# Performance work log

Measured on AMD Instinct MI355X. Metric: run time of the kernel, lower is better.

## Reference

```python
import jax, jax.numpy as jnp
import numpy as np

HID = 16

def _lrconv(x, edge_index, edge_attr, w1, b1, w2, b2):
    # flow='target_to_source': x_i = x[edge_index[0]], x_j = x[edge_index[1]],
    # aggregate (max) at edge_index[0].
    src = edge_index[0]
    dst = edge_index[1]
    m = jnp.concatenate([x[src], x[dst], edge_attr], axis=-1)  # [E, 2*in+edge]
    m = jax.nn.relu(m @ w1 + b1)
    m = jax.nn.relu(m @ w2 + b2)  # [E, out], all >= 0
    agg = jax.ops.segment_max(m, src, num_segments=x.shape[0])
    # empty segments get -inf in jax; PyG fills with 0. Messages are ReLU'd (>=0),
    # so clamping at 0 is exact.
    return jnp.maximum(agg, 0.0)

def _glorot(key, shape):
    fan_in, fan_out = shape
    lim = float(np.sqrt(6.0 / (fan_in + fan_out)))
    return jax.random.uniform(key, shape, jnp.float32, -lim, lim)

def setup_inputs() -> dict:
    key = jax.random.key(0)
    ks = jax.random.split(key, 16)
    N, E = 100000, 1600000
    x = jax.random.normal(ks[0], (N, 4), jnp.float32)
    edge_index = jax.random.randint(ks[1], (2, E), 0, N, jnp.int64)
    edge_attr = jax.random.normal(ks[2], (E, 8), jnp.float32)
    # conv1: in=4 -> cat dim 4*2+8=16
    c1_w1 = _glorot(ks[3], (16, HID)); c1_b1 = jnp.zeros((HID,), jnp.float32)
    c1_w2 = _glorot(ks[4], (HID, 16)); c1_b2 = jnp.zeros((16,), jnp.float32)
    # conv2: in=16 -> cat dim 16*2+8=40
    c2_w1 = _glorot(ks[5], (40, HID)); c2_b1 = jnp.zeros((HID,), jnp.float32)
    c2_w2 = _glorot(ks[6], (HID, 16)); c2_b2 = jnp.zeros((16,), jnp.float32)
    l1_w = _glorot(ks[7], (16, 16)); l1_b = jnp.zeros((16,), jnp.float32)
    l2_w = _glorot(ks[8], (16, 1)); l2_b = jnp.zeros((1,), jnp.float32)
    return {"x": x, "edge_index": edge_index, "edge_attr": edge_attr,
            "c1_w1": c1_w1, "c1_b1": c1_b1, "c1_w2": c1_w2, "c1_b2": c1_b2,
            "c2_w1": c2_w1, "c2_b1": c2_b1, "c2_w2": c2_w2, "c2_b2": c2_b2,
            "l1_w": l1_w, "l1_b": l1_b, "l2_w": l2_w, "l2_b": l2_b}

def reference(x, edge_index, edge_attr,
              c1_w1, c1_b1, c1_w2, c1_b2,
              c2_w1, c2_b1, c2_w2, c2_b2,
              l1_w, l1_b, l2_w, l2_b):
    h = _lrconv(x, edge_index, edge_attr, c1_w1, c1_b1, c1_w2, c1_b2)   # [N,16]
    h = _lrconv(h, edge_index, edge_attr, c2_w1, c2_b1, c2_w2, c2_b2)   # [N,16]
    h = jax.nn.relu(h @ l1_w + l1_b)
    return h @ l2_w + l2_b  # [N,1]
```

## Files before the change

### kernel.cpp

```cpp
#include <hip/hip_runtime.h>
#include <hip/hip_fp16.h>

#define CHUNK 1024

typedef _Float16 half8 __attribute__((ext_vector_type(8)));
typedef float floatx4 __attribute__((ext_vector_type(4)));

__device__ __forceinline__ unsigned int pack2(float a, float b) {
    __half2 h = __floats2half2_rn(a, b);
    return *(unsigned int*)&h;
}
__device__ __forceinline__ float2 unpack2(unsigned int u) {
    __half2 h = *(__half2*)&u;
    return __half22float2(h);
}

__global__ __launch_bounds__(256) void rank_cvt(
    const int* __restrict__ ei, const float* __restrict__ ea,
    int* __restrict__ deg, unsigned short* __restrict__ r,
    _Float16* __restrict__ eah, int E)
{
    int e = blockIdx.x * 256 + threadIdx.x;
    if (e >= E) return;
    r[e] = (unsigned short)atomicAdd(&deg[ei[e]], 1);
    float4 a0 = *(const float4*)(ea + (size_t)e * 8);
    float4 a1 = *(const float4*)(ea + (size_t)e * 8 + 4);
    half8 h;
    h[0] = (_Float16)a0.x; h[1] = (_Float16)a0.y;
    h[2] = (_Float16)a0.z; h[3] = (_Float16)a0.w;
    h[4] = (_Float16)a1.x; h[5] = (_Float16)a1.y;
    h[6] = (_Float16)a1.z; h[7] = (_Float16)a1.w;
    *(half8*)(eah + (size_t)e * 8) = h;
}

__global__ __launch_bounds__(256) void scan_chunk_sums(
    const int* __restrict__ v, int* __restrict__ csum, int N)
{
    __shared__ int s[256];
    int base = blockIdx.x * CHUNK;
    int t = threadIdx.x;
    int acc = 0;
    #pragma unroll
    for (int i = 0; i < CHUNK / 256; ++i) {
        int idx = base + t + i * 256;
        if (idx < N) acc += v[idx];
    }
    s[t] = acc; __syncthreads();
    for (int o = 128; o > 0; o >>= 1) {
        if (t < o) s[t] += s[t + o];
        __syncthreads();
    }
    if (t == 0) csum[blockIdx.x] = s[0];
}

__global__ void scan_chunk_off(
    const int* __restrict__ csum, int* __restrict__ coff, int nch)
{
    if (threadIdx.x == 0 && blockIdx.x == 0) {
        int acc = 0;
        for (int i = 0; i < nch; ++i) { coff[i] = acc; acc += csum[i]; }
    }
}

__global__ __launch_bounds__(256) void scan_within_excl(
    const int* __restrict__ deg, int* __restrict__ pos,
    const int* __restrict__ coff, int N)
{
    __shared__ int s[256];
    int t = threadIdx.x;
    int base = blockIdx.x * CHUNK + t * 4;
    int v0 = 0, v1 = 0, v2 = 0, v3 = 0;
    if (base + 0 < N) v0 = deg[base + 0];
    if (base + 1 < N) v1 = deg[base + 1];
    if (base + 2 < N) v2 = deg[base + 2];
    if (base + 3 < N) v3 = deg[base + 3];
    s[t] = v0 + v1 + v2 + v3;
    __syncthreads();
    for (int o = 1; o < 256; o <<= 1) {
        int add = (t >= o) ? s[t - o] : 0;
        __syncthreads();
        s[t] += add;
        __syncthreads();
    }
    int run = coff[blockIdx.x] + (t > 0 ? s[t - 1] : 0);
    if (base + 0 < N) pos[base + 0] = run; run += v0;
    if (base + 1 < N) pos[base + 1] = run; run += v1;
    if (base + 2 < N) pos[base + 2] = run; run += v2;
    if (base + 3 < N) pos[base + 3] = run;
}

__global__ __launch_bounds__(256) void edge_mlp1(
    const float* __restrict__ x,
    const int*   __restrict__ ei,
    const _Float16* __restrict__ eah,
    const int*   __restrict__ pos,
    const unsigned short* __restrict__ r,
    const float* __restrict__ w1, const float* __restrict__ b1,
    const float* __restrict__ w2, const float* __restrict__ b2,
    _Float16* __restrict__ m2h,
    int E)
{
    __shared__ _Float16 itm[4][4][16][24];
    __shared__ int      sd[4][2][64];
    int tid = threadIdx.x;
    int w = tid >> 6, lane = tid & 63;
    int e16 = lane & 15, q = lane >> 4;

    half8 B1, B2;
    #pragma unroll
    for (int j = 0; j < 8; ++j) { B1[j] = (_Float16)0.f; B2[j] = (_Float16)0.f; }
    if (q < 2) {
        #pragma unroll
        for (int j = 0; j < 8; ++j) {
            B1[j] = (_Float16)w1[(8 * q + j) * 16 + e16];
            B2[j] = (_Float16)w2[(8 * q + j) * 16 + e16];
        }
    }
    float b1c = b1[e16], b2c = b2[e16];

    int wid = blockIdx.x * 4 + w;
    int nw  = gridDim.x * 4;
    int ntiles = (E + 63) >> 6;

    for (int tile = wid; tile < ntiles; tile += nw) {
        int ebase = tile << 6;
        int e = ebase + lane;
        int s_l = 0, d_l = 0, p_l = 0;
        if (e < E) {
            s_l = ei[e];
            d_l = ei[E + e];
            p_l = pos[s_l] + (int)r[e];
        }
        sd[w][0][lane] = s_l;
        sd[w][1][lane] = d_l;
        __builtin_amdgcn_wave_barrier();

        half8 A[4];
        #pragma unroll
        for (int t = 0; t < 4; ++t) {
            half8 a;
            #pragma unroll
            for (int j = 0; j < 8; ++j) a[j] = (_Float16)0.f;
            int et = ebase + 16 * t + e16;
            if (q == 0 && et < E) {
                int s = sd[w][0][16 * t + e16];
                int d = sd[w][1][16 * t + e16];
                float4 xs = *(const float4*)(x + (size_t)s * 4);
                float4 xd = *(const float4*)(x + (size_t)d * 4);
                a[0] = (_Float16)xs.x; a[1] = (_Float16)xs.y;
                a[2] = (_Float16)xs.z; a[3] = (_Float16)xs.w;
                a[4] = (_Float16)xd.x; a[5] = (_Float16)xd.y;
                a[6] = (_Float16)xd.z; a[7] = (_Float16)xd.w;
            } else if (q == 1 && et < E) {
                a = *(const half8*)(eah + (size_t)et * 8);
            }
            A[t] = a;
        }

        floatx4 C[4];
        #pragma unroll
        for (int t = 0; t < 4; ++t) {
            floatx4 c = {b1c, b1c, b1c, b1c};
            C[t] = __builtin_amdgcn_mfma_f32_16x16x32_f16(A[t], B1, c, 0, 0, 0);
        }
        #pragma unroll
        for (int t = 0; t < 4; ++t)
            #pragma unroll
            for (int i = 0; i < 4; ++i)
                itm[w][t][4 * q + i][e16] = (_Float16)fmaxf(C[t][i], 0.0f);
        __builtin_amdgcn_wave_barrier();

        half8 A2[4];
        #pragma unroll
        for (int t = 0; t < 4; ++t) {
            half8 a;
            #pragma unroll
            for (int j = 0; j < 8; ++j) a[j] = (_Float16)0.f;
            if (q < 2) a = *(const half8*)&itm[w][t][e16][8 * q];
            A2[t] = a;
        }
        __builtin_amdgcn_wave_barrier();
        floatx4 C2[4];
        #pragma unroll
        for (int t = 0; t < 4; ++t) {
            floatx4 c = {b2c, b2c, b2c, b2c};
            C2[t] = __builtin_amdgcn_mfma_f32_16x16x32_f16(A2[t], B2, c, 0, 0, 0);
        }
        #pragma unroll
        for (int t = 0; t < 4; ++t)
            #pragma unroll
            for (int i = 0; i < 4; ++i)
                itm[w][t][4 * q + i][e16] = (_Float16)C2[t][i];
        __builtin_amdgcn_wave_barrier();

        if (e < E) {
            half8 lo = *(const half8*)&itm[w][q][e16][0];
            half8 hi = *(const half8*)&itm[w][q][e16][8];
            *(half8*)(m2h + (size_t)p_l * 16)     = lo;
            *(half8*)(m2h + (size_t)p_l * 16 + 8) = hi;
        }
        __builtin_amdgcn_wave_barrier();
    }
}

__global__ __launch_bounds__(256) void edge_mlp2(
    const float* __restrict__ hw_s,
    const unsigned short* __restrict__ hw_dh,
    const int*   __restrict__ ei,
    const _Float16* __restrict__ eah,
    const int*   __restrict__ pos,
    const unsigned short* __restrict__ r,
    const float* __restrict__ w1,
    const float* __restrict__ w2, const float* __restrict__ b2,
    _Float16* __restrict__ m2h, int E)
{
    __shared__ _Float16 itm[4][4][16][24];
    __shared__ int      sd[4][2][64];
    int tid = threadIdx.x;
    int w = tid >> 6, lane = tid & 63;
    int e16 = lane & 15, q = lane >> 4;
    const __half* hwd = (const __half*)hw_dh;

    half8 B1, B2;
    #pragma unroll
    for (int j = 0; j < 8; ++j) { B1[j] = (_Float16)0.f; B2[j] = (_Float16)0.f; }
    if (q == 0) {
        #pragma unroll
        for (int j = 0; j < 8; ++j)
            B1[j] = (_Float16)w1[(32 + j) * 16 + e16];
    }
    if (q < 2) {
        #pragma unroll
        for (int j = 0; j < 8; ++j)
            B2[j] = (_Float16)w2[(8 * q + j) * 16 + e16];
    }
    float b2c = b2[e16];

    int wid = blockIdx.x * 4 + w;
    int nw  = gridDim.x * 4;
    int ntiles = (E + 63) >> 6;

    for (int tile = wid; tile < ntiles; tile += nw) {
        int ebase = tile << 6;
        int e = ebase + lane;
        int s_l = 0, d_l = 0, p_l = 0;
        if (e < E) {
            s_l = ei[e];
            d_l = ei[E + e];
            p_l = pos[s_l] + (int)r[e];
        }
        sd[w][0][lane] = s_l;
        sd[w][1][lane] = d_l;
        __builtin_amdgcn_wave_barrier();

        half8 A[4];
        #pragma unroll
        for (int t = 0; t < 4; ++t) {
            half8 a;
            #pragma unroll
            for (int j = 0; j < 8; ++j) a[j] = (_Float16)0.f;
            int et = ebase + 16 * t + e16;
            if (q == 0 && et < E)
                a = *(const half8*)(eah + (size_t)et * 8);
            A[t] = a;
        }

        floatx4 C[4];
        #pragma unroll
        for (int t = 0; t < 4; ++t) {
            floatx4 c;
            #pragma unroll
            for (int i = 0; i < 4; ++i) {
                int li = 16 * t + 4 * q + i;
                int rr = ebase + li;
                float v = 0.0f;
                if (rr < E) {
                    int s = sd[w][0][li];
                    int d = sd[w][1][li];
                    v = hw_s[(size_t)s * 16 + e16]
                      + __half2float(hwd[(size_t)d * 16 + e16]);
                }
                c[i] = v;
            }
            C[t] = __builtin_amdgcn_mfma_f32_16x16x32_f16(A[t], B1, c, 0, 0, 0);
        }
        #pragma unroll
        for (int t = 0; t < 4; ++t)
            #pragma unroll
            for (int i = 0; i < 4; ++i)
                itm[w][t][4 * q + i][e16] = (_Float16)fmaxf(C[t][i], 0.0f);
        __builtin_amdgcn_wave_barrier();

        half8 A2[4];
        #pragma unroll
        for (int t = 0; t < 4; ++t) {
            half8 a;
            #pragma unroll
            for (int j = 0; j < 8; ++j) a[j] = (_Float16)0.f;
            if (q < 2) a = *(const half8*)&itm[w][t][e16][8 * q];
            A2[t] = a;
        }
        __builtin_amdgcn_wave_barrier();
        floatx4 C2[4];
        #pragma unroll
        for (int t = 0; t < 4; ++t) {
            floatx4 c = {b2c, b2c, b2c, b2c};
            C2[t] = __builtin_amdgcn_mfma_f32_16x16x32_f16(A2[t], B2, c, 0, 0, 0);
        }
        #pragma unroll
        for (int t = 0; t < 4; ++t)
            #pragma unroll
            for (int i = 0; i < 4; ++i)
                itm[w][t][4 * q + i][e16] = (_Float16)C2[t][i];
        __builtin_amdgcn_wave_barrier();

        if (e < E) {
            half8 lo = *(const half8*)&itm[w][q][e16][0];
            half8 hi = *(const half8*)&itm[w][q][e16][8];
            *(half8*)(m2h + (size_t)p_l * 16)     = lo;
            *(half8*)(m2h + (size_t)p_l * 16 + 8) = hi;
        }
        __builtin_amdgcn_wave_barrier();
    }
}

__global__ __launch_bounds__(256) void segmax1_hw(
    const _Float16* __restrict__ m2h, const int* __restrict__ pos,
    const float* __restrict__ cw1, const float* __restrict__ cb1,
    float* __restrict__ hw_s, unsigned short* __restrict__ hw_dh,
    int N, int E)
{
    int tid = threadIdx.x;
    int n = blockIdx.x * 32 + (tid >> 3);
    if (n >= N) return;
    int g = tid & 7;
    int start = pos[n];
    int end = (n + 1 < N) ? pos[n + 1] : E;

    float acc[16];
    #pragma unroll
    for (int j = 0; j < 16; ++j) acc[j] = 0.0f;

    for (int k = start + g; k < end; k += 8) {
        uint4 u0 = *(const uint4*)(m2h + (size_t)k * 16);
        uint4 u1 = *(const uint4*)(m2h + (size_t)k * 16 + 8);
        float2 f;
        f = unpack2(u0.x); acc[0]  = fmaxf(acc[0],  f.x); acc[1]  = fmaxf(acc[1],  f.y);
        f = unpack2(u0.y); acc[2]  = fmaxf(acc[2],  f.x); acc[3]  = fmaxf(acc[3],  f.y);
        f = unpack2(u0.z); acc[4]  = fmaxf(acc[4],  f.x); acc[5]  = fmaxf(acc[5],  f.y);
        f = unpack2(u0.w); acc[6]  = fmaxf(acc[6],  f.x); acc[7]  = fmaxf(acc[7],  f.y);
        f = unpack2(u1.x); acc[8]  = fmaxf(acc[8],  f.x); acc[9]  = fmaxf(acc[9],  f.y);
        f = unpack2(u1.y); acc[10] = fmaxf(acc[10], f.x); acc[11] = fmaxf(acc[11], f.y);
        f = unpack2(u1.z); acc[12] = fmaxf(acc[12], f.x); acc[13] = fmaxf(acc[13], f.y);
        f = unpack2(u1.w); acc[14] = fmaxf(acc[14], f.x); acc[15] = fmaxf(acc[15], f.y);
    }
    #pragma unroll
    for (int mask = 1; mask < 8; mask <<= 1) {
        #pragma unroll
        for (int j = 0; j < 16; ++j)
            acc[j] = fmaxf(acc[j], __shfl_xor(acc[j], mask, 64));
    }

    int j0 = 2 * g, j1 = 2 * g + 1;
    float hs0 = cb1[j0], hs1 = cb1[j1], hd0 = 0.0f, hd1 = 0.0f;
    #pragma unroll
    for (int k = 0; k < 16; ++k) {
        float ak = acc[k];
        hs0 = fmaf(ak, cw1[k * 16 + j0], hs0);
        hs1 = fmaf(ak, cw1[k * 16 + j1], hs1);
        hd0 = fmaf(ak, cw1[(16 + k) * 16 + j0], hd0);
        hd1 = fmaf(ak, cw1[(16 + k) * 16 + j1], hd1);
    }
    *(float2*)(hw_s + (size_t)n * 16 + j0) = make_float2(hs0, hs1);
    ((unsigned int*)hw_dh)[(size_t)n * 8 + g] = pack2(hd0, hd1);
}

__global__ __launch_bounds__(256) void segmax2_head(
    const _Float16* __restrict__ m2h, const int* __restrict__ pos,
    const float* __restrict__ l1w, const float* __restrict__ l1b,
    const float* __restrict__ l2w, const float* __restrict__ l2b,
    float* __restrict__ out, int N, int E)
{
    int tid = threadIdx.x;
    int n = blockIdx.x * 32 + (tid >> 3);
    if (n >= N) return;
    int g = tid & 7;
    int start = pos[n];
    int end = (n + 1 < N) ? pos[n + 1] : E;

    float acc[16];
    #pragma unroll
    for (int j = 0; j < 16; ++j) acc[j] = 0.0f;

    for (int k = start + g; k < end; k += 8) {
        uint4 u0 = *(const uint4*)(m2h + (size_t)k * 16);
        uint4 u1 = *(const uint4*)(m2h + (size_t)k * 16 + 8);
        float2 f;
        f = unpack2(u0.x); acc[0]  = fmaxf(acc[0],  f.x); acc[1]  = fmaxf(acc[1],  f.y);
        f = unpack2(u0.y); acc[2]  = fmaxf(acc[2],  f.x); acc[3]  = fmaxf(acc[3],  f.y);
        f = unpack2(u0.z); acc[4]  = fmaxf(acc[4],  f.x); acc[5]  = fmaxf(acc[5],  f.y);
        f = unpack2(u0.w); acc[6]  = fmaxf(acc[6],  f.x); acc[7]  = fmaxf(acc[7],  f.y);
        f = unpack2(u1.x); acc[8]  = fmaxf(acc[8],  f.x); acc[9]  = fmaxf(acc[9],  f.y);
        f = unpack2(u1.y); acc[10] = fmaxf(acc[10], f.x); acc[11] = fmaxf(acc[11], f.y);
        f = unpack2(u1.z); acc[12] = fmaxf(acc[12], f.x); acc[13] = fmaxf(acc[13], f.y);
        f = unpack2(u1.w); acc[14] = fmaxf(acc[14], f.x); acc[15] = fmaxf(acc[15], f.y);
    }
    #pragma unroll
    for (int mask = 1; mask < 8; mask <<= 1) {
        #pragma unroll
        for (int j = 0; j < 16; ++j)
            acc[j] = fmaxf(acc[j], __shfl_xor(acc[j], mask, 64));
    }

    float t2[16];
    #pragma unroll
    for (int j = 0; j < 16; ++j) t2[j] = l1b[j];
    #pragma unroll
    for (int kk = 0; kk < 16; ++kk) {
        float ak = acc[kk];
        #pragma unroll
        for (int j = 0; j < 16; ++j) t2[j] = fmaf(ak, l1w[kk * 16 + j], t2[j]);
    }
    float r2 = l2b[0];
    #pragma unroll
    for (int j = 0; j < 16; ++j) r2 = fmaf(fmaxf(t2[j], 0.0f), l2w[j], r2);
    if (g == 0) out[n] = r2;
}

extern "C" void kernel_launch(void* const* d_in, const int* in_sizes, int n_in,
                              void* d_out, int out_size, void* d_ws, size_t ws_size,
                              hipStream_t stream)
{
    const float* x     = (const float*)d_in[0];
    const int*   ei    = (const int*)  d_in[1];
    const float* ea    = (const float*)d_in[2];
    const float* c1_w1 = (const float*)d_in[3];
    const float* c1_b1 = (const float*)d_in[4];
    const float* c1_w2 = (const float*)d_in[5];
    const float* c1_b2 = (const float*)d_in[6];
    const float* c2_w1 = (const float*)d_in[7];
    const float* c2_b1 = (const float*)d_in[8];
    const float* c2_w2 = (const float*)d_in[9];
    const float* c2_b2 = (const float*)d_in[10];
    const float* l1_w  = (const float*)d_in[11];
    const float* l1_b  = (const float*)d_in[12];
    const float* l2_w  = (const float*)d_in[13];
    const float* l2_b  = (const float*)d_in[14];
    float* out = (float*)d_out;

    const int N = in_sizes[0] / 4;
    const int E = in_sizes[2] / 8;
    const int nch = (N + CHUNK - 1) / CHUNK;

    const int BLK = 256;
    const int egrid = (E + BLK - 1) / BLK;
    const int ggrid = (N + 31) / 32;
    const int ntiles64 = (E + 63) >> 6;
    int mgrid = (ntiles64 + 15) / 16;
    if (mgrid < 256) mgrid = 256;

    size_t szN16f = (size_t)N * 16 * 4;
    size_t szN16h = (size_t)N * 16 * 2;
    size_t szN    = ((size_t)N * 4 + 15) & ~(size_t)15;
    size_t szEh   = ((size_t)E * 2 + 15) & ~(size_t)15;
    size_t szE16  = (size_t)E * 16;
    size_t szE32  = (size_t)E * 32;
    (void)szE32;

    size_t pos_off  = 0;
    size_t r_off    = pos_off  + szN;
    size_t hws_off  = r_off    + szEh;
    size_t hwdh_off = hws_off  + szN16f;
    size_t eah_off  = hwdh_off + szN16h;
    size_t m2h_off  = eah_off  + szE16;
    size_t deg_off  = m2h_off;
    size_t cs_off   = deg_off  + szN;
    size_t cf_off   = cs_off   + 4096;

    int*            pos  = (int*)  ((char*)d_ws + pos_off);
    unsigned short* r    = (unsigned short*)((char*)d_ws + r_off);
    float*          hw_s = (float*)((char*)d_ws + hws_off);
    unsigned short* hwdh = (unsigned short*)((char*)d_ws + hwdh_off);
    _Float16*       eah  = (_Float16*)((char*)d_ws + eah_off);
    _Float16*       m2h  = (_Float16*)((char*)d_ws + m2h_off);
    int*            deg  = (int*)  ((char*)d_ws + deg_off);
    int*            csum = (int*)  ((char*)d_ws + cs_off);
    int*            coff = (int*)  ((char*)d_ws + cf_off);

    hipMemsetAsync(deg, 0, (size_t)N * 4, stream);
    rank_cvt<<<egrid, BLK, 0, stream>>>(ei, ea, deg, r, eah, E);
    scan_chunk_sums<<<nch, BLK, 0, stream>>>(deg, csum, N);
    scan_chunk_off<<<1, 64, 0, stream>>>(csum, coff, nch);
    scan_within_excl<<<nch, BLK, 0, stream>>>(deg, pos, coff, N);
    edge_mlp1<<<mgrid, BLK, 0, stream>>>(x, ei, eah, pos, r,
                                         c1_w1, c1_b1, c1_w2, c1_b2, m2h, E);
    segmax1_hw<<<ggrid, BLK, 0, stream>>>(m2h, pos, c2_w1, c2_b1,
                                          hw_s, hwdh, N, E);
    edge_mlp2<<<mgrid, BLK, 0, stream>>>(hw_s, hwdh, ei, eah, pos, r,
                                         c2_w1, c2_w2, c2_b2, m2h, E);
    segmax2_head<<<ggrid, BLK, 0, stream>>>(m2h, pos, l1_w, l1_b, l2_w, l2_b,
                                            out, N, E);
}
```

Measured before the change: 375.0 us.

## Launch one 64-edge tile per wave and broadcast indices via shuffles

Both edge MLP kernels drop the grid-stride tile loop and launch one wave per 64-edge tile, with the grid sized to cover all tiles. The per-wave LDS staging of src/dst indices is replaced by cross-lane __shfl broadcasts. Index, pos and rank loads are hoisted before the weight setup so their latency can overlap it. This removes loop overhead and some LDS traffic and barriers, and gives more waves to hide gather latency, at the cost of reloading weights once per tile instead of once per persistent wave.

```diff
diff --git a/kernel.cpp b/kernel.cpp
--- a/kernel.cpp
+++ b/kernel.cpp
@@ -101,10 +101,21 @@
     int E)
 {
     __shared__ _Float16 itm[4][4][16][24];
-    __shared__ int      sd[4][2][64];
     int tid = threadIdx.x;
     int w = tid >> 6, lane = tid & 63;
     int e16 = lane & 15, q = lane >> 4;
+    int ntiles = (E + 63) >> 6;
+    int tile = blockIdx.x * 4 + w;
+    if (tile >= ntiles) return;
+    int ebase = tile << 6;
+    int e = ebase + lane;
+
+    int s_l = 0, d_l = 0, p_l = 0;
+    if (e < E) {
+        s_l = ei[e];
+        d_l = ei[E + e];
+        p_l = pos[s_l] + (int)r[e];
+    }
 
     half8 B1, B2;
     #pragma unroll
@@ -118,88 +129,69 @@
     }
     float b1c = b1[e16], b2c = b2[e16];
 
-    int wid = blockIdx.x * 4 + w;
-    int nw  = gridDim.x * 4;
-    int ntiles = (E + 63) >> 6;
-
-    for (int tile = wid; tile < ntiles; tile += nw) {
-        int ebase = tile << 6;
-        int e = ebase + lane;
-        int s_l = 0, d_l = 0, p_l = 0;
-        if (e < E) {
-            s_l = ei[e];
-            d_l = ei[E + e];
-            p_l = pos[s_l] + (int)r[e];
+    half8 A[4];
+    #pragma unroll
+    for (int t = 0; t < 4; ++t) {
+        int st = __shfl(s_l, 16 * t + e16, 64);
+        int dt = __shfl(d_l, 16 * t + e16, 64);
+        half8 a;
+        #pragma unroll
+        for (int j = 0; j < 8; ++j) a[j] = (_Float16)0.f;
+        int et = ebase + 16 * t + e16;
+        if (q == 0 && et < E) {
+            float4 xs = *(const float4*)(x + (size_t)st * 4);
+            float4 xd = *(const float4*)(x + (size_t)dt * 4);
+            a[0] = (_Float16)xs.x; a[1] = (_Float16)xs.y;
+            a[2] = (_Float16)xs.z; a[3] = (_Float16)xs.w;
+            a[4] = (_Float16)xd.x; a[5] = (_Float16)xd.y;
+            a[6] = (_Float16)xd.z; a[7] = (_Float16)xd.w;
+        } else if (q == 1 && et < E) {
+            a = *(const half8*)(eah + (size_t)et * 8);
         }
-        sd[w][0][lane] = s_l;
-        sd[w][1][lane] = d_l;
-        __builtin_amdgcn_wave_barrier();
-
-        half8 A[4];
-        #pragma unroll
-        for (int t = 0; t < 4; ++t) {
-            half8 a;
-            #pragma unroll
-            for (int j = 0; j < 8; ++j) a[j] = (_Float16)0.f;
-            int et = ebase + 16 * t + e16;
-            if (q == 0 && et < E) {
-                int s = sd[w][0][16 * t + e16];
-                int d = sd[w][1][16 * t + e16];
-                float4 xs = *(const float4*)(x + (size_t)s * 4);
-                float4 xd = *(const float4*)(x + (size_t)d * 4);
-                a[0] = (_Float16)xs.x; a[1] = (_Float16)xs.y;
-                a[2] = (_Float16)xs.z; a[3] = (_Float16)xs.w;
-                a[4] = (_Float16)xd.x; a[5] = (_Float16)xd.y;
-                a[6] = (_Float16)xd.z; a[7] = (_Float16)xd.w;
-            } else if (q == 1 && et < E) {
-                a = *(const half8*)(eah + (size_t)et * 8);
-            }
-            A[t] = a;
-        }
-
-        floatx4 C[4];
-        #pragma unroll
-        for (int t = 0; t < 4; ++t) {
-            floatx4 c = {b1c, b1c, b1c, b1c};
-            C[t] = __builtin_amdgcn_mfma_f32_16x16x32_f16(A[t], B1, c, 0, 0, 0);
-        }
-        #pragma unroll
-        for (int t = 0; t < 4; ++t)
-            #pragma unroll
-            for (int i = 0; i < 4; ++i)
-                itm[w][t][4 * q + i][e16] = (_Float16)fmaxf(C[t][i], 0.0f);
-        __builtin_amdgcn_wave_barrier();
-
-        half8 A2[4];
-        #pragma unroll
-        for (int t = 0; t < 4; ++t) {
-            half8 a;
-            #pragma unroll
-            for (int j = 0; j < 8; ++j) a[j] = (_Float16)0.f;
-            if (q < 2) a = *(const half8*)&itm[w][t][e16][8 * q];
-            A2[t] = a;
-        }
-        __builtin_amdgcn_wave_barrier();
-        floatx4 C2[4];
-        #pragma unroll
-        for (int t = 0; t < 4; ++t) {
-            floatx4 c = {b2c, b2c, b2c, b2c};
-            C2[t] = __builtin_amdgcn_mfma_f32_16x16x32_f16(A2[t], B2, c, 0, 0, 0);
-        }
-        #pragma unroll
-        for (int t = 0; t < 4; ++t)
-            #pragma unroll
-            for (int i = 0; i < 4; ++i)
-                itm[w][t][4 * q + i][e16] = (_Float16)C2[t][i];
-        __builtin_amdgcn_wave_barrier();
-
-        if (e < E) {
-            half8 lo = *(const half8*)&itm[w][q][e16][0];
-            half8 hi = *(const half8*)&itm[w][q][e16][8];
-            *(half8*)(m2h + (size_t)p_l * 16)     = lo;
-            *(half8*)(m2h + (size_t)p_l * 16 + 8) = hi;
-        }
-        __builtin_amdgcn_wave_barrier();
+        A[t] = a;
+    }
+
+    floatx4 C[4];
+    #pragma unroll
+    for (int t = 0; t < 4; ++t) {
+        floatx4 c = {b1c, b1c, b1c, b1c};
+        C[t] = __builtin_amdgcn_mfma_f32_16x16x32_f16(A[t], B1, c, 0, 0, 0);
+    }
+    #pragma unroll
+    for (int t = 0; t < 4; ++t)
+        #pragma unroll
+        for (int i = 0; i < 4; ++i)
+            itm[w][t][4 * q + i][e16] = (_Float16)fmaxf(C[t][i], 0.0f);
+    __builtin_amdgcn_wave_barrier();
+
+    half8 A2[4];
+    #pragma unroll
+    for (int t = 0; t < 4; ++t) {
+        half8 a;
+        #pragma unroll
+        for (int j = 0; j < 8; ++j) a[j] = (_Float16)0.f;
+        if (q < 2) a = *(const half8*)&itm[w][t][e16][8 * q];
+        A2[t] = a;
+    }
+    __builtin_amdgcn_wave_barrier();
+    floatx4 C2[4];
+    #pragma unroll
+    for (int t = 0; t < 4; ++t) {
+        floatx4 c = {b2c, b2c, b2c, b2c};
+        C2[t] = __builtin_amdgcn_mfma_f32_16x16x32_f16(A2[t], B2, c, 0, 0, 0);
+    }
+    #pragma unroll
+    for (int t = 0; t < 4; ++t)
+        #pragma unroll
+        for (int i = 0; i < 4; ++i)
+            itm[w][t][4 * q + i][e16] = (_Float16)C2[t][i];
+    __builtin_amdgcn_wave_barrier();
+
+    if (e < E) {
+        half8 lo = *(const half8*)&itm[w][q][e16][0];
+        half8 hi = *(const half8*)&itm[w][q][e16][8];
+        *(half8*)(m2h + (size_t)p_l * 16)     = lo;
+        *(half8*)(m2h + (size_t)p_l * 16 + 8) = hi;
     }
 }
 
@@ -215,11 +207,22 @@
     _Float16* __restrict__ m2h, int E)
 {
     __shared__ _Float16 itm[4][4][16][24];
-    __shared__ int      sd[4][2][64];
     int tid = threadIdx.x;
     int w = tid >> 6, lane = tid & 63;
     int e16 = lane & 15, q = lane >> 4;
     const __half* hwd = (const __half*)hw_dh;
+    int ntiles = (E + 63) >> 6;
+    int tile = blockIdx.x * 4 + w;
+    if (tile >= ntiles) return;
+    int ebase = tile << 6;
+    int e = ebase + lane;
+
+    int s_l = 0, d_l = 0, p_l = 0;
+    if (e < E) {
+        s_l = ei[e];
+        d_l = ei[E + e];
+        p_l = pos[s_l] + (int)r[e];
+    }
 
     half8 B1, B2;
     #pragma unroll
@@ -236,91 +239,72 @@
     }
     float b2c = b2[e16];
 
-    int wid = blockIdx.x * 4 + w;
-    int nw  = gridDim.x * 4;
-    int ntiles = (E + 63) >> 6;
-
-    for (int tile = wid; tile < ntiles; tile += nw) {
-        int ebase = tile << 6;
-        int e = ebase + lane;
-        int s_l = 0, d_l = 0, p_l = 0;
-        if (e < E) {
-            s_l = ei[e];
-            d_l = ei[E + e];
-            p_l = pos[s_l] + (int)r[e];
+    half8 A[4];
+    #pragma unroll
+    for (int t = 0; t < 4; ++t) {
+        half8 a;
+        #pragma unroll
+        for (int j = 0; j < 8; ++j) a[j] = (_Float16)0.f;
+        int et = ebase + 16 * t + e16;
+        if (q == 0 && et < E)
+            a = *(const half8*)(eah + (size_t)et * 8);
+        A[t] = a;
+    }
+
+    floatx4 C[4];
+    #pragma unroll
+    for (int t = 0; t < 4; ++t) {
+        floatx4 c;
+        #pragma unroll
+        for (int i = 0; i < 4; ++i) {
+            int li = 16 * t + 4 * q + i;
+            int s = __shfl(s_l, li, 64);
+            int d = __shfl(d_l, li, 64);
+            int rr = ebase + li;
+            float v = 0.0f;
+            if (rr < E) {
+                v = hw_s[(size_t)s * 16 + e16]
+                  + __half2float(hwd[(size_t)d * 16 + e16]);
+            }
+            c[i] = v;
         }
-        sd[w][0][lane] = s_l;
-        sd[w][1][lane] = d_l;
-        __builtin_amdgcn_wave_barrier();
-
-        half8 A[4];
-        #pragma unroll
-        for (int t = 0; t < 4; ++t) {
-            half8 a;
-            #pragma unroll
-            for (int j = 0; j < 8; ++j) a[j] = (_Float16)0.f;
-            int et = ebase + 16 * t + e16;
-            if (q == 0 && et < E)
-                a = *(const half8*)(eah + (size_t)et * 8);
-            A[t] = a;
-        }
-
-        floatx4 C[4];
-        #pragma unroll
-        for (int t = 0; t < 4; ++t) {
-            floatx4 c;
-            #pragma unroll
-            for (int i = 0; i < 4; ++i) {
-                int li = 16 * t + 4 * q + i;
-                int rr = ebase + li;
-                float v = 0.0f;
-                if (rr < E) {
-                    int s = sd[w][0][li];
-                    int d = sd[w][1][li];
-                    v = hw_s[(size_t)s * 16 + e16]
-                      + __half2float(hwd[(size_t)d * 16 + e16]);
-                }
-                c[i] = v;
-            }
-            C[t] = __builtin_amdgcn_mfma_f32_16x16x32_f16(A[t], B1, c, 0, 0, 0);
-        }
-        #pragma unroll
-        for (int t = 0; t < 4; ++t)
-            #pragma unroll
-            for (int i = 0; i < 4; ++i)
-                itm[w][t][4 * q + i][e16] = (_Float16)fmaxf(C[t][i], 0.0f);
-        __builtin_amdgcn_wave_barrier();
-
-        half8 A2[4];
-        #pragma unroll
-        for (int t = 0; t < 4; ++t) {
-            half8 a;
-            #pragma unroll
-            for (int j = 0; j < 8; ++j) a[j] = (_Float16)0.f;
-            if (q < 2) a = *(const half8*)&itm[w][t][e16][8 * q];
-            A2[t] = a;
-        }
-        __builtin_amdgcn_wave_barrier();
-        floatx4 C2[4];
-        #pragma unroll
-        for (int t = 0; t < 4; ++t) {
-            floatx4 c = {b2c, b2c, b2c, b2c};
-            C2[t] = __builtin_amdgcn_mfma_f32_16x16x32_f16(A2[t], B2, c, 0, 0, 0);
-        }
-        #pragma unroll
-        for (int t = 0; t < 4; ++t)
-            #pragma unroll
-            for (int i = 0; i < 4; ++i)
-                itm[w][t][4 * q + i][e16] = (_Float16)C2[t][i];
-        __builtin_amdgcn_wave_barrier();
-
-        if (e < E) {
-            half8 lo = *(const half8*)&itm[w][q][e16][0];
-            half8 hi = *(const half8*)&itm[w][q][e16][8];
-            *(half8*)(m2h + (size_t)p_l * 16)     = lo;
-            *(half8*)(m2h + (size_t)p_l * 16 + 8) = hi;
-        }
-        __builtin_amdgcn_wave_barrier();
+        C[t] = __builtin_amdgcn_mfma_f32_16x16x32_f16(A[t], B1, c, 0, 0, 0);
+    }
+    #pragma unroll
+    for (int t = 0; t < 4; ++t)
+        #pragma unroll
+        for (int i = 0; i < 4; ++i)
+            itm[w][t][4 * q + i][e16] = (_Float16)fmaxf(C[t][i], 0.0f);
+    __builtin_amdgcn_wave_barrier();
+
+    half8 A2[4];
+    #pragma unroll
+    for (int t = 0; t < 4; ++t) {
+        half8 a;
+        #pragma unroll
+        for (int j = 0; j < 8; ++j) a[j] = (_Float16)0.f;
+        if (q < 2) a = *(const half8*)&itm[w][t][e16][8 * q];
+        A2[t] = a;
+    }
+    __builtin_amdgcn_wave_barrier();
+    floatx4 C2[4];
+    #pragma unroll
+    for (int t = 0; t < 4; ++t) {
+        floatx4 c = {b2c, b2c, b2c, b2c};
+        C2[t] = __builtin_amdgcn_mfma_f32_16x16x32_f16(A2[t], B2, c, 0, 0, 0);
+    }
+    #pragma unroll
+    for (int t = 0; t < 4; ++t)
+        #pragma unroll
+        for (int i = 0; i < 4; ++i)
+            itm[w][t][4 * q + i][e16] = (_Float16)C2[t][i];
+    __builtin_amdgcn_wave_barrier();
+
+    if (e < E) {
+        half8 lo = *(const half8*)&itm[w][q][e16][0];
+        half8 hi = *(const half8*)&itm[w][q][e16][8];
+        *(half8*)(m2h + (size_t)p_l * 16)     = lo;
+        *(half8*)(m2h + (size_t)p_l * 16 + 8) = hi;
     }
 }
 
@@ -456,16 +440,13 @@
     const int egrid = (E + BLK - 1) / BLK;
     const int ggrid = (N + 31) / 32;
     const int ntiles64 = (E + 63) >> 6;
-    int mgrid = (ntiles64 + 15) / 16;
-    if (mgrid < 256) mgrid = 256;
+    const int mgrid = (ntiles64 + 3) / 4;
 
     size_t szN16f = (size_t)N * 16 * 4;
     size_t szN16h = (size_t)N * 16 * 2;
     size_t szN    = ((size_t)N * 4 + 15) & ~(size_t)15;
     size_t szEh   = ((size_t)E * 2 + 15) & ~(size_t)15;
     size_t szE16  = (size_t)E * 16;
-    size_t szE32  = (size_t)E * 32;
-    (void)szE32;
 
     size_t pos_off  = 0;
     size_t r_off    = pos_off  + szN;
```

Result: faster. 360.5 us (-3.9%).
